# Kernel optimization log

Hardware: AMD Instinct MI355X
Metric: run time of the kernel (lower is better)

The kernel has to match this reference:

```python
import jax, jax.numpy as jnp
import numpy as np

NUM_HEADS = 8
CATEGORY_SIZE = 128


def setup_inputs() -> dict:
    key = jax.random.key(0)
    k0, k1, k2 = jax.random.split(key, 3)
    b, n, c, t = 4, 16384, 256, 64
    qkv = jax.random.normal(k0, (b, n, 3 * c), dtype=jnp.float32)
    sim = jax.random.normal(k1, (b, n, t), dtype=jnp.float32)
    proj_w = jax.random.normal(k2, (c, c), dtype=jnp.float32) * 0.02
    proj_b = jnp.zeros((c,), dtype=jnp.float32)
    logit_scale = jnp.log(10.0 * jnp.ones((1, 1), dtype=jnp.float32))
    return {"qkv": qkv, "sim": sim, "proj_w": proj_w, "proj_b": proj_b,
            "logit_scale": logit_scale, "h": 128, "w": 128}


def reference(qkv, sim, proj_w, proj_b, logit_scale, h, w):
    b, n, c3 = qkv.shape
    c = c3 // 3
    hds = NUM_HEADS
    d = c // hds
    gs = min(n, CATEGORY_SIZE)
    ng = (n + gs - 1) // gs
    pad_n = ng * gs - n

    # category id per token, sort tokens by category
    tk_id = jnp.argmax(sim, axis=-1)                      # [b, n]
    sort_idx = jnp.argsort(tk_id, axis=-1)                # [b, n]
    rev_idx = jnp.argsort(sort_idx, axis=-1)              # inverse permutation (== index_reverse)

    shuf = jnp.take_along_axis(qkv, sort_idx[:, :, None], axis=1)  # [b, n, 3c]
    if pad_n > 0:
        pad = jnp.flip(shuf[:, n - pad_n:n, :], axis=1)
        shuf = jnp.concatenate([shuf, pad], axis=1)

    # [b, ng, gs, 3, hds, d] -> (3, b, ng, hds, gs, d)
    qkv_g = shuf.reshape(b, ng, gs, 3, hds, d)
    qkv_g = jnp.transpose(qkv_g, (3, 0, 1, 4, 2, 5))
    q, k, v = qkv_g[0], qkv_g[1], qkv_g[2]

    max_log = jnp.log(jnp.asarray(1.0 / 0.01, dtype=logit_scale.dtype))
    scale = jnp.exp(jnp.minimum(logit_scale, max_log))    # clamp then exp, shape (1,1)

    attn = jnp.einsum('bghqd,bghkd->bghqk', q, k) * scale  # [b, ng, hds, gs, gs]
    attn = jax.nn.softmax(attn, axis=-1)
    y = jnp.einsum('bghqk,bghkd->bghqd', attn, v)           # [b, ng, hds, gs, d]

    y = jnp.transpose(y, (0, 1, 3, 2, 4)).reshape(b, n + pad_n, c)[:, :n, :]
    x = jnp.take_along_axis(y, rev_idx[:, :, None], axis=1)  # scatter back
    return x @ proj_w.T + proj_b
```

## Files before the change

kernel.cpp:

```cpp
#include <hip/hip_runtime.h>

#define BB   4
#define NN   16384
#define CC   256
#define TT   64
#define HH   8
#define DD   32
#define GSZ  128
#define NGR  128

typedef __attribute__((ext_vector_type(8))) short s16x8;
typedef __attribute__((ext_vector_type(4))) float f32x4;

__device__ __forceinline__ unsigned short f2bf(float f) {
  unsigned int u = __float_as_uint(f);
  u += 0x7FFFu + ((u >> 16) & 1u);
  return (unsigned short)(u >> 16);
}

__global__ __launch_bounds__(256) void cat_hist_kernel(
    const float* __restrict__ sim, int* __restrict__ cat, int* __restrict__ hist)
{
  const int idx = blockIdx.x * 256 + threadIdx.x;
  const float4* row = (const float4*)(sim + (size_t)idx * TT);
  float best = -3.4e38f; int bi = 0;
  #pragma unroll
  for (int j = 0; j < TT / 4; j++) {
    float4 v = row[j];
    if (v.x > best) { best = v.x; bi = j * 4 + 0; }
    if (v.y > best) { best = v.y; bi = j * 4 + 1; }
    if (v.z > best) { best = v.z; bi = j * 4 + 2; }
    if (v.w > best) { best = v.w; bi = j * 4 + 3; }
  }
  cat[idx] = bi;
  atomicAdd(&hist[((idx >> 14) << 6) + bi], 1);
}

__global__ void prefix_kernel(const int* __restrict__ hist, int* __restrict__ catStart)
{
  int b = threadIdx.x;
  if (b < BB) {
    int acc = 0;
    for (int c = 0; c < TT; c++) { catStart[b * TT + c] = acc; acc += hist[b * TT + c]; }
  }
}

__global__ __launch_bounds__(256) void sort_positions_kernel(
    const int* __restrict__ cat, const int* __restrict__ catStart, int* __restrict__ srcOf)
{
  const int b = blockIdx.x >> 6;
  const int c = blockIdx.x & 63;
  const int* catb = cat + (size_t)b * NN;
  const int tid = threadIdx.x;
  const int beg = tid * (NN / 256);
  int cnt = 0;
  for (int i = 0; i < NN / 256; i++) cnt += (catb[beg + i] == c);
  __shared__ int sc[256];
  sc[tid] = cnt; __syncthreads();
  for (int off = 1; off < 256; off <<= 1) {
    int v = (tid >= off) ? sc[tid - off] : 0;
    __syncthreads();
    sc[tid] += v;
    __syncthreads();
  }
  int pos = catStart[(b << 6) + c] + sc[tid] - cnt;
  int* dst = srcOf + (size_t)b * NN;
  for (int i = 0; i < NN / 256; i++) {
    int t = beg + i;
    if (catb[t] == c) dst[pos++] = t;
  }
}

__global__ __launch_bounds__(256) void attn_kernel(
    const float* __restrict__ qkv, const int* __restrict__ srcOf,
    const float* __restrict__ lsp, unsigned short* __restrict__ xb)
{
  __shared__ float Qt[DD][GSZ];
  __shared__ float Kt[DD][GSZ];
  __shared__ float Vt[DD][GSZ];
  __shared__ int srcL[GSZ];

  const int bid = blockIdx.x;
  const int h = bid & 7;
  const int g = (bid >> 3) & (NGR - 1);
  const int b = bid >> 10;
  const int tid = threadIdx.x;

  const float scale = __expf(fminf(lsp[0], 4.6051702f));

  if (tid < GSZ) srcL[tid] = srcOf[b * NN + g * GSZ + tid];
  __syncthreads();

  {
    const int tok = tid >> 1;
    const int fh = (tid & 1) * 16;
    const float* bp = qkv + ((size_t)(b * NN + srcL[tok])) * (3 * CC) + h * DD + fh;
    #pragma unroll
    for (int u = 0; u < 4; u++) {
      float4 q4 = *(const float4*)(bp + u * 4);
      float4 k4 = *(const float4*)(bp + CC + u * 4);
      float4 v4 = *(const float4*)(bp + 2 * CC + u * 4);
      int d = fh + u * 4;
      Qt[d + 0][tok] = q4.x * scale; Qt[d + 1][tok] = q4.y * scale;
      Qt[d + 2][tok] = q4.z * scale; Qt[d + 3][tok] = q4.w * scale;
      Kt[d + 0][tok] = k4.x; Kt[d + 1][tok] = k4.y;
      Kt[d + 2][tok] = k4.z; Kt[d + 3][tok] = k4.w;
      Vt[d + 0][tok] = v4.x; Vt[d + 1][tok] = v4.y;
      Vt[d + 2][tok] = v4.z; Vt[d + 3][tok] = v4.w;
    }
  }
  __syncthreads();

  const int rg = tid >> 3, cg = tid & 7;
  const int r0 = rg * 4, c0 = cg * 16;

  float s[4][16];
  #pragma unroll
  for (int r = 0; r < 4; r++)
    #pragma unroll
    for (int t = 0; t < 16; t++) s[r][t] = 0.f;

  #pragma unroll 4
  for (int i = 0; i < DD; i++) {
    float4 q4 = *(const float4*)&Qt[i][r0];
    float qr[4] = {q4.x, q4.y, q4.z, q4.w};
    float4 ka = *(const float4*)&Kt[i][c0];
    float4 kb2 = *(const float4*)&Kt[i][c0 + 4];
    float4 kc2 = *(const float4*)&Kt[i][c0 + 8];
    float4 kd2 = *(const float4*)&Kt[i][c0 + 12];
    float kk[16] = {ka.x, ka.y, ka.z, ka.w, kb2.x, kb2.y, kb2.z, kb2.w,
                    kc2.x, kc2.y, kc2.z, kc2.w, kd2.x, kd2.y, kd2.z, kd2.w};
    #pragma unroll
    for (int r = 0; r < 4; r++)
      #pragma unroll
      for (int t = 0; t < 16; t++)
        s[r][t] = fmaf(qr[r], kk[t], s[r][t]);
  }

  float m[4], l[4], inv[4];
  #pragma unroll
  for (int r = 0; r < 4; r++) {
    float mm = -3.4e38f;
    #pragma unroll
    for (int t = 0; t < 16; t++) mm = fmaxf(mm, s[r][t]);
    mm = fmaxf(mm, __shfl_xor(mm, 1));
    mm = fmaxf(mm, __shfl_xor(mm, 2));
    mm = fmaxf(mm, __shfl_xor(mm, 4));
    m[r] = mm;
  }
  #pragma unroll
  for (int r = 0; r < 4; r++) {
    float acc = 0.f;
    #pragma unroll
    for (int t = 0; t < 16; t++) {
      float e = __expf(s[r][t] - m[r]);
      s[r][t] = e; acc += e;
    }
    acc += __shfl_xor(acc, 1);
    acc += __shfl_xor(acc, 2);
    acc += __shfl_xor(acc, 4);
    l[r] = acc;
    inv[r] = 1.0f / acc;
  }

  #pragma unroll 1
  for (int ps = 0; ps < 4; ps++) {
    const int d0 = ps * 8;
    float y[4][8];
    #pragma unroll
    for (int r = 0; r < 4; r++)
      #pragma unroll
      for (int j = 0; j < 8; j++) y[r][j] = 0.f;

    #pragma unroll
    for (int j = 0; j < 8; j++) {
      float4 va = *(const float4*)&Vt[d0 + j][c0];
      float4 vb3 = *(const float4*)&Vt[d0 + j][c0 + 4];
      float4 vc3 = *(const float4*)&Vt[d0 + j][c0 + 8];
      float4 vd3 = *(const float4*)&Vt[d0 + j][c0 + 12];
      float vv[16] = {va.x, va.y, va.z, va.w, vb3.x, vb3.y, vb3.z, vb3.w,
                      vc3.x, vc3.y, vc3.z, vc3.w, vd3.x, vd3.y, vd3.z, vd3.w};
      #pragma unroll
      for (int r = 0; r < 4; r++) {
        float acc = y[r][j];
        #pragma unroll
        for (int t = 0; t < 16; t++) acc = fmaf(s[r][t], vv[t], acc);
        y[r][j] = acc;
      }
    }
    #pragma unroll
    for (int r = 0; r < 4; r++)
      #pragma unroll
      for (int j = 0; j < 8; j++) {
        y[r][j] += __shfl_xor(y[r][j], 1);
        y[r][j] += __shfl_xor(y[r][j], 2);
        y[r][j] += __shfl_xor(y[r][j], 4);
      }
    if (cg == 0) {
      #pragma unroll
      for (int r = 0; r < 4; r++) {
        const int row = r0 + r;
        const int src = srcL[row];
        s16x8 pk;
        #pragma unroll
        for (int j = 0; j < 8; j++) pk[j] = (short)f2bf(y[r][j] * inv[r]);
        *(s16x8*)&xb[((size_t)(b * NN + src)) * CC + h * DD + d0] = pk;
      }
    }
  }
}

__global__ __launch_bounds__(256) void proj_kernel(
    const unsigned short* __restrict__ xb, const float* __restrict__ W,
    const float* __restrict__ bias, float* __restrict__ out)
{
  const int tid = threadIdx.x;
  const int wave = tid >> 6;
  const int lane = tid & 63;
  const int n0 = wave * 64;
  const int lr = lane & 15;
  const int kb = lane >> 4;

  s16x8 wf[4][8];
  #pragma unroll
  for (int nt = 0; nt < 4; nt++)
    #pragma unroll
    for (int ks = 0; ks < 8; ks++) {
      const float* wp = W + (size_t)(n0 + nt * 16 + lr) * CC + ks * 32 + kb * 8;
      float4 w0 = *(const float4*)wp;
      float4 w1 = *(const float4*)(wp + 4);
      s16x8 wv;
      wv[0] = (short)f2bf(w0.x); wv[1] = (short)f2bf(w0.y);
      wv[2] = (short)f2bf(w0.z); wv[3] = (short)f2bf(w0.w);
      wv[4] = (short)f2bf(w1.x); wv[5] = (short)f2bf(w1.y);
      wv[6] = (short)f2bf(w1.z); wv[7] = (short)f2bf(w1.w);
      wf[nt][ks] = wv;
    }
  float bs[4];
  #pragma unroll
  for (int nt = 0; nt < 4; nt++) bs[nt] = bias[n0 + nt * 16 + lr];

  const int MT = (BB * NN) / 16;
  for (int mt = blockIdx.x; mt < MT; mt += gridDim.x) {
    const int m0 = mt * 16;
    const unsigned short* xrow = xb + (size_t)(m0 + lr) * CC + kb * 8;
    s16x8 a[8];
    #pragma unroll
    for (int ks = 0; ks < 8; ks++) a[ks] = *(const s16x8*)(xrow + ks * 32);
    #pragma unroll
    for (int nt = 0; nt < 4; nt++) {
      f32x4 acc = {0.f, 0.f, 0.f, 0.f};
      #pragma unroll
      for (int ks = 0; ks < 8; ks++)
        acc = __builtin_amdgcn_mfma_f32_16x16x32_bf16(a[ks], wf[nt][ks], acc, 0, 0, 0);
      const int ccol = n0 + nt * 16 + lr;
      #pragma unroll
      for (int q = 0; q < 4; q++) {
        const int row = m0 + kb * 4 + q;
        out[(size_t)row * CC + ccol] = acc[q] + bs[nt];
      }
    }
  }
}

extern "C" void kernel_launch(void* const* d_in, const int* in_sizes, int n_in,
                              void* d_out, int out_size, void* d_ws, size_t ws_size,
                              hipStream_t stream)
{
  (void)in_sizes; (void)n_in; (void)out_size; (void)ws_size;
  const float* qkv  = (const float*)d_in[0];
  const float* sim  = (const float*)d_in[1];
  const float* W    = (const float*)d_in[2];
  const float* bias = (const float*)d_in[3];
  const float* lsp  = (const float*)d_in[4];
  float* out = (float*)d_out;

  char* ws = (char*)d_ws;
  unsigned short* xb = (unsigned short*)ws;
  size_t off = (size_t)BB * NN * CC * sizeof(unsigned short);
  int* srcOf = (int*)(ws + off); off += (size_t)BB * NN * sizeof(int);
  int* cat   = (int*)(ws + off); off += (size_t)BB * NN * sizeof(int);
  int* hist  = (int*)(ws + off); off += (size_t)BB * TT * sizeof(int);
  int* catStart = (int*)(ws + off);

  hipMemsetAsync(hist, 0, BB * TT * sizeof(int), stream);
  cat_hist_kernel<<<(BB * NN) / 256, 256, 0, stream>>>(sim, cat, hist);
  prefix_kernel<<<1, 64, 0, stream>>>(hist, catStart);
  sort_positions_kernel<<<BB * TT, 256, 0, stream>>>(cat, catStart, srcOf);
  attn_kernel<<<BB * NGR * HH, 256, 0, stream>>>(qkv, srcOf, lsp, xb);
  proj_kernel<<<512, 256, 0, stream>>>(xb, W, bias, out);
}
```

Baseline: 552.4 us.

## Use bf16 MFMA with split-precision QK^T in attention kernel

Rewrites the per-group attention to use 32x32x16 bf16 MFMA instructions in place of scalar FP32 FMAs. QK^T keeps near-fp32 accuracy by splitting Q and K into high and low bf16 parts and issuing three MFMAs per step. Softmax probabilities are packed to bf16 and multiplied against V held in a swizzled bf16 LDS tile. Q and K are loaded straight from global into registers, which cuts shared memory use but adds conversion work and lowers PV precision to bf16.

```diff
diff --git a/kernel.cpp b/kernel.cpp
--- a/kernel.cpp
+++ b/kernel.cpp
@@ -11,11 +11,29 @@
 
 typedef __attribute__((ext_vector_type(8))) short s16x8;
 typedef __attribute__((ext_vector_type(4))) float f32x4;
+typedef __attribute__((ext_vector_type(16))) float f32x16;
+typedef __attribute__((ext_vector_type(4))) unsigned int u32x4;
+
+union FragU { u32x4 u; s16x8 s; };
 
 __device__ __forceinline__ unsigned short f2bf(float f) {
   unsigned int u = __float_as_uint(f);
   u += 0x7FFFu + ((u >> 16) & 1u);
   return (unsigned short)(u >> 16);
+}
+
+__device__ __forceinline__ unsigned int cvtpk_bf16(float a, float b) {
+  unsigned int r;
+  asm("v_cvt_pk_bf16_f32 %0, %1, %2" : "=v"(r) : "v"(a), "v"(b));
+  return r;
+}
+
+__device__ __forceinline__ void split2(float a, float b,
+                                       unsigned int& wh, unsigned int& wl) {
+  wh = cvtpk_bf16(a, b);
+  float ra = __uint_as_float(wh << 16);
+  float rb = __uint_as_float(wh & 0xffff0000u);
+  wl = cvtpk_bf16(a - ra, b - rb);
 }
 
 __global__ __launch_bounds__(256) void cat_hist_kernel(
@@ -75,138 +93,138 @@
     const float* __restrict__ qkv, const int* __restrict__ srcOf,
     const float* __restrict__ lsp, unsigned short* __restrict__ xb)
 {
-  __shared__ float Qt[DD][GSZ];
-  __shared__ float Kt[DD][GSZ];
-  __shared__ float Vt[DD][GSZ];
-  __shared__ int srcL[GSZ];
+  __shared__ int srcLs[GSZ];
+  __shared__ unsigned short VtL[DD * GSZ];
 
   const int bid = blockIdx.x;
-  const int h = bid & 7;
+  const int hH = bid & 7;
   const int g = (bid >> 3) & (NGR - 1);
   const int b = bid >> 10;
   const int tid = threadIdx.x;
+  const int lane = tid & 63;
+  const int wid = tid >> 6;
+  const int ql = lane & 31;
+  const int hf = lane >> 5;
 
   const float scale = __expf(fminf(lsp[0], 4.6051702f));
-
-  if (tid < GSZ) srcL[tid] = srcOf[b * NN + g * GSZ + tid];
+  const float* qkvB = qkv + (size_t)b * NN * (3 * CC);
+
+  if (tid < GSZ) srcLs[tid] = srcOf[b * NN + g * GSZ + tid];
   __syncthreads();
 
   {
-    const int tok = tid >> 1;
-    const int fh = (tid & 1) * 16;
-    const float* bp = qkv + ((size_t)(b * NN + srcL[tok])) * (3 * CC) + h * DD + fh;
-    #pragma unroll
-    for (int u = 0; u < 4; u++) {
-      float4 q4 = *(const float4*)(bp + u * 4);
-      float4 k4 = *(const float4*)(bp + CC + u * 4);
-      float4 v4 = *(const float4*)(bp + 2 * CC + u * 4);
-      int d = fh + u * 4;
-      Qt[d + 0][tok] = q4.x * scale; Qt[d + 1][tok] = q4.y * scale;
-      Qt[d + 2][tok] = q4.z * scale; Qt[d + 3][tok] = q4.w * scale;
-      Kt[d + 0][tok] = k4.x; Kt[d + 1][tok] = k4.y;
-      Kt[d + 2][tok] = k4.z; Kt[d + 3][tok] = k4.w;
-      Vt[d + 0][tok] = v4.x; Vt[d + 1][tok] = v4.y;
-      Vt[d + 2][tok] = v4.z; Vt[d + 3][tok] = v4.w;
-    }
-  }
+    const int tp = tid & 63;
+    const int o = tid >> 6;
+    const int t0 = srcLs[2 * tp], t1 = srcLs[2 * tp + 1];
+    const float* v0p = qkvB + (size_t)t0 * (3 * CC) + 2 * CC + hH * DD + 8 * o;
+    const float* v1p = qkvB + (size_t)t1 * (3 * CC) + 2 * CC + hH * DD + 8 * o;
+    float4 a0 = *(const float4*)v0p, a1 = *(const float4*)(v0p + 4);
+    float4 b0 = *(const float4*)v1p, b1 = *(const float4*)(v1p + 4);
+    float va[8] = {a0.x, a0.y, a0.z, a0.w, a1.x, a1.y, a1.z, a1.w};
+    float vb[8] = {b0.x, b0.y, b0.z, b0.w, b1.x, b1.y, b1.z, b1.w};
+    #pragma unroll
+    for (int u = 0; u < 8; u++) {
+      const int dim = 8 * o + u;
+      unsigned int val = cvtpk_bf16(va[u], vb[u]);
+      const int byte = dim * 256 + ((((tp >> 2) ^ (dim & 15))) << 4) + ((4 * tp) & 15);
+      *(unsigned int*)((char*)VtL + byte) = val;
+    }
+  }
+
+  const int tokQ = srcLs[32 * wid + ql];
+  FragU qh[2], qlo[2];
+  {
+    const float* qp = qkvB + (size_t)tokQ * (3 * CC) + hH * DD;
+    #pragma unroll
+    for (int ks = 0; ks < 2; ks++) {
+      const float* p8 = qp + 16 * ks + 8 * hf;
+      float4 f0 = *(const float4*)p8, f1 = *(const float4*)(p8 + 4);
+      float f[8] = {f0.x * scale, f0.y * scale, f0.z * scale, f0.w * scale,
+                    f1.x * scale, f1.y * scale, f1.z * scale, f1.w * scale};
+      #pragma unroll
+      for (int c = 0; c < 4; c++) {
+        unsigned int wh, wl;
+        split2(f[2 * c], f[2 * c + 1], wh, wl);
+        qh[ks].u[c] = wh; qlo[ks].u[c] = wl;
+      }
+    }
+  }
+
   __syncthreads();
 
-  const int rg = tid >> 3, cg = tid & 7;
-  const int r0 = rg * 4, c0 = cg * 16;
-
-  float s[4][16];
-  #pragma unroll
-  for (int r = 0; r < 4; r++)
-    #pragma unroll
-    for (int t = 0; t < 16; t++) s[r][t] = 0.f;
-
-  #pragma unroll 4
-  for (int i = 0; i < DD; i++) {
-    float4 q4 = *(const float4*)&Qt[i][r0];
-    float qr[4] = {q4.x, q4.y, q4.z, q4.w};
-    float4 ka = *(const float4*)&Kt[i][c0];
-    float4 kb2 = *(const float4*)&Kt[i][c0 + 4];
-    float4 kc2 = *(const float4*)&Kt[i][c0 + 8];
-    float4 kd2 = *(const float4*)&Kt[i][c0 + 12];
-    float kk[16] = {ka.x, ka.y, ka.z, ka.w, kb2.x, kb2.y, kb2.z, kb2.w,
-                    kc2.x, kc2.y, kc2.z, kc2.w, kd2.x, kd2.y, kd2.z, kd2.w};
-    #pragma unroll
-    for (int r = 0; r < 4; r++)
+  f32x16 accS[4];
+  #pragma unroll
+  for (int mt = 0; mt < 4; mt++) {
+    #pragma unroll
+    for (int r = 0; r < 16; r++) accS[mt][r] = 0.f;
+    const int tokK = srcLs[32 * mt + ql];
+    const float* kp = qkvB + (size_t)tokK * (3 * CC) + CC + hH * DD;
+    #pragma unroll
+    for (int ks = 0; ks < 2; ks++) {
+      const float* p8 = kp + 16 * ks + 8 * hf;
+      float4 f0 = *(const float4*)p8, f1 = *(const float4*)(p8 + 4);
+      float f[8] = {f0.x, f0.y, f0.z, f0.w, f1.x, f1.y, f1.z, f1.w};
+      FragU kh, kl;
       #pragma unroll
-      for (int t = 0; t < 16; t++)
-        s[r][t] = fmaf(qr[r], kk[t], s[r][t]);
-  }
-
-  float m[4], l[4], inv[4];
-  #pragma unroll
-  for (int r = 0; r < 4; r++) {
-    float mm = -3.4e38f;
-    #pragma unroll
-    for (int t = 0; t < 16; t++) mm = fmaxf(mm, s[r][t]);
-    mm = fmaxf(mm, __shfl_xor(mm, 1));
-    mm = fmaxf(mm, __shfl_xor(mm, 2));
-    mm = fmaxf(mm, __shfl_xor(mm, 4));
-    m[r] = mm;
-  }
-  #pragma unroll
-  for (int r = 0; r < 4; r++) {
-    float acc = 0.f;
-    #pragma unroll
-    for (int t = 0; t < 16; t++) {
-      float e = __expf(s[r][t] - m[r]);
-      s[r][t] = e; acc += e;
-    }
-    acc += __shfl_xor(acc, 1);
-    acc += __shfl_xor(acc, 2);
-    acc += __shfl_xor(acc, 4);
-    l[r] = acc;
-    inv[r] = 1.0f / acc;
-  }
-
-  #pragma unroll 1
-  for (int ps = 0; ps < 4; ps++) {
-    const int d0 = ps * 8;
-    float y[4][8];
-    #pragma unroll
-    for (int r = 0; r < 4; r++)
-      #pragma unroll
-      for (int j = 0; j < 8; j++) y[r][j] = 0.f;
-
-    #pragma unroll
-    for (int j = 0; j < 8; j++) {
-      float4 va = *(const float4*)&Vt[d0 + j][c0];
-      float4 vb3 = *(const float4*)&Vt[d0 + j][c0 + 4];
-      float4 vc3 = *(const float4*)&Vt[d0 + j][c0 + 8];
-      float4 vd3 = *(const float4*)&Vt[d0 + j][c0 + 12];
-      float vv[16] = {va.x, va.y, va.z, va.w, vb3.x, vb3.y, vb3.z, vb3.w,
-                      vc3.x, vc3.y, vc3.z, vc3.w, vd3.x, vd3.y, vd3.z, vd3.w};
-      #pragma unroll
-      for (int r = 0; r < 4; r++) {
-        float acc = y[r][j];
-        #pragma unroll
-        for (int t = 0; t < 16; t++) acc = fmaf(s[r][t], vv[t], acc);
-        y[r][j] = acc;
+      for (int c = 0; c < 4; c++) {
+        unsigned int wh, wl;
+        split2(f[2 * c], f[2 * c + 1], wh, wl);
+        kh.u[c] = wh; kl.u[c] = wl;
       }
-    }
-    #pragma unroll
-    for (int r = 0; r < 4; r++)
-      #pragma unroll
-      for (int j = 0; j < 8; j++) {
-        y[r][j] += __shfl_xor(y[r][j], 1);
-        y[r][j] += __shfl_xor(y[r][j], 2);
-        y[r][j] += __shfl_xor(y[r][j], 4);
-      }
-    if (cg == 0) {
-      #pragma unroll
-      for (int r = 0; r < 4; r++) {
-        const int row = r0 + r;
-        const int src = srcL[row];
-        s16x8 pk;
-        #pragma unroll
-        for (int j = 0; j < 8; j++) pk[j] = (short)f2bf(y[r][j] * inv[r]);
-        *(s16x8*)&xb[((size_t)(b * NN + src)) * CC + h * DD + d0] = pk;
-      }
-    }
+      accS[mt] = __builtin_amdgcn_mfma_f32_32x32x16_bf16(kh.s, qh[ks].s,  accS[mt], 0, 0, 0);
+      accS[mt] = __builtin_amdgcn_mfma_f32_32x32x16_bf16(kh.s, qlo[ks].s, accS[mt], 0, 0, 0);
+      accS[mt] = __builtin_amdgcn_mfma_f32_32x32x16_bf16(kl.s, qh[ks].s,  accS[mt], 0, 0, 0);
+    }
+  }
+
+  float mx = -3.4e38f;
+  #pragma unroll
+  for (int mt = 0; mt < 4; mt++)
+    #pragma unroll
+    for (int r = 0; r < 16; r++) mx = fmaxf(mx, accS[mt][r]);
+  mx = fmaxf(mx, __shfl_xor(mx, 32));
+
+  float sm = 0.f;
+  unsigned int w[4][8];
+  #pragma unroll
+  for (int mt = 0; mt < 4; mt++) {
+    float p[16];
+    #pragma unroll
+    for (int r = 0; r < 16; r++) { p[r] = __expf(accS[mt][r] - mx); sm += p[r]; }
+    #pragma unroll
+    for (int c = 0; c < 8; c++) w[mt][c] = cvtpk_bf16(p[2 * c], p[2 * c + 1]);
+  }
+  sm += __shfl_xor(sm, 32);
+  const float inv = 1.0f / sm;
+
+  f32x16 accY;
+  #pragma unroll
+  for (int r = 0; r < 16; r++) accY[r] = 0.f;
+  const int vrow = ql;
+  #pragma unroll
+  for (int ks = 0; ks < 8; ks++) {
+    const int mt = ks >> 1, hh = ks & 1;
+    unsigned int send0 = hf ? w[mt][4 * hh + 0] : w[mt][4 * hh + 2];
+    unsigned int send1 = hf ? w[mt][4 * hh + 1] : w[mt][4 * hh + 3];
+    unsigned int f0 = __shfl_xor(send0, 32);
+    unsigned int f1 = __shfl_xor(send1, 32);
+    FragU pb;
+    pb.u[0] = hf ? f0 : w[mt][4 * hh + 0];
+    pb.u[1] = hf ? f1 : w[mt][4 * hh + 1];
+    pb.u[2] = hf ? w[mt][4 * hh + 2] : f0;
+    pb.u[3] = hf ? w[mt][4 * hh + 3] : f1;
+    const int byte = vrow * 256 + (((2 * ks + hf) ^ (vrow & 15)) << 4);
+    s16x8 vfrag = *(s16x8*)((char*)VtL + byte);
+    accY = __builtin_amdgcn_mfma_f32_32x32x16_bf16(vfrag, pb.s, accY, 0, 0, 0);
+  }
+
+  unsigned short* orow = xb + ((size_t)(b * NN + tokQ)) * CC + hH * DD;
+  #pragma unroll
+  for (int rq = 0; rq < 4; rq++) {
+    unsigned int u0 = cvtpk_bf16(accY[4 * rq + 0] * inv, accY[4 * rq + 1] * inv);
+    unsigned int u1 = cvtpk_bf16(accY[4 * rq + 2] * inv, accY[4 * rq + 3] * inv);
+    const int dim0 = 8 * rq + 4 * hf;
+    *(uint2*)(orow + dim0) = make_uint2(u0, u1);
   }
 }
 
@@ -283,7 +301,7 @@
   int* hist  = (int*)(ws + off); off += (size_t)BB * TT * sizeof(int);
   int* catStart = (int*)(ws + off);
 
-  hipMemsetAsync(hist, 0, BB * TT * sizeof(int), stream);
+  (void)hipMemsetAsync(hist, 0, BB * TT * sizeof(int), stream);
   cat_hist_kernel<<<(BB * NN) / 256, 256, 0, stream>>>(sim, cat, hist);
   prefix_kernel<<<1, 64, 0, stream>>>(hist, catStart);
   sort_positions_kernel<<<BB * TT, 256, 0, stream>>>(cat, catStart, srcOf);
```

Measured after the change: 442.3 us. 1.25x faster.
